# Performance work log

Hardware: AMD Instinct MI355X
Metric: run time of the kernel (lower is better)

## Reference

```python
import jax, jax.numpy as jnp
import numpy as np
from jax import lax

EMBED = 200
HID = 300
NCLASS = 2
B = 64
S = 255          # complete binary tree: 2**8 - 1 nodes
DEPTH = 8        # levels 0..7, root at node 0
VOCAB = 32000


def make_tree():
    parent = np.zeros(S, np.int32)
    parent[0] = S  # sentinel: root has no parent (dropped via dummy segment)
    for i in range(1, S):
        parent[i] = (i - 1) // 2
    depth = np.floor(np.log2(np.arange(S) + 1)).astype(np.int32)
    return jnp.asarray(parent), jnp.asarray(depth)


def setup_inputs() -> dict:
    key = jax.random.key(0)
    ks = jax.random.split(key, 8)
    parent, depth = make_tree()
    return {
        "x": jax.random.randint(ks[0], (S, B), 0, VOCAB, dtype=jnp.int32),
        "parent": parent,
        "depth": depth,
        "embed": jax.random.normal(ks[1], (VOCAB, EMBED), jnp.float32) * 0.1,
        "W_iou": jax.random.normal(ks[2], (EMBED, 3 * HID), jnp.float32) * 0.05,
        "U_iou": jax.random.normal(ks[3], (HID, 3 * HID), jnp.float32) * 0.05,
        "b_iou": jnp.zeros((3 * HID,), jnp.float32),
        "W_f": jax.random.normal(ks[4], (EMBED, HID), jnp.float32) * 0.05,
        "U_f": jax.random.normal(ks[5], (HID, HID), jnp.float32) * 0.05,
        "b_f": jnp.zeros((HID,), jnp.float32),
        "W_out": jax.random.normal(ks[6], (HID, NCLASS), jnp.float32) * 0.05,
        "b_out": jnp.zeros((NCLASS,), jnp.float32),
    }


def reference(x, parent, depth, embed, W_iou, U_iou, b_iou, W_f, U_f, b_f, W_out, b_out):
    # x: [S, B] token ids (seq-major, as in the torch model)
    emb = embed[x]                              # [S, B, E]
    wx_iou = emb @ W_iou + b_iou                # [S, B, 3H] input contributions
    wx_f = emb @ W_f + b_f                      # [S, B, H]
    seg = jnp.minimum(parent, S)                # root -> dummy segment S
    pidx = jnp.clip(parent, 0, S - 1)           # safe gather index for parent's x-part

    H0 = jnp.zeros((S, B, HID), emb.dtype)
    C0 = jnp.zeros((S, B, HID), emb.dtype)

    def level_step(carry, d):
        H, C = carry
        child = (depth == d + 1)[:, None, None].astype(H.dtype)   # nodes feeding level d
        # child-sum of hidden states into parents
        h_sum = jax.ops.segment_sum(H * child, seg, num_segments=S + 1)[:S]  # [S,B,H]
        # per-child forget gate: sigma(W_f x_parent + U_f h_child + b_f)
        f = jax.nn.sigmoid(wx_f[pidx] + H @ U_f)                  # [S,B,H]
        fc = jax.ops.segment_sum(f * C * child, seg, num_segments=S + 1)[:S]
        iou = wx_iou + h_sum @ U_iou                              # [S,B,3H]
        i_g, o_g, u_g = jnp.split(iou, 3, axis=-1)
        i_g = jax.nn.sigmoid(i_g)
        o_g = jax.nn.sigmoid(o_g)
        u_g = jnp.tanh(u_g)
        c_new = i_g * u_g + fc
        h_new = o_g * jnp.tanh(c_new)
        node = (depth == d)[:, None, None]
        H = jnp.where(node, h_new, H)
        C = jnp.where(node, c_new, C)
        return (H, C), None

    levels = jnp.arange(DEPTH - 1, -1, -1)      # process deepest level first
    (H, C), _ = lax.scan(level_step, (H0, C0), levels)

    tree_hidden = H[0]                          # [B, H] root hidden state
    logits = tree_hidden @ W_out + b_out        # Linear(hidden_dim, n_class)
    return jax.nn.log_softmax(logits, axis=-1)  # [B, 2]
```

## Files before the change

kernel.cpp:

```cpp
#include <hip/hip_runtime.h>
#include <hip/hip_bf16.h>
#include <math.h>

#define NS 255
#define NB 64
#define NE 200
#define NH 300
#define TS 2048


typedef __attribute__((ext_vector_type(8))) short short8;
typedef __attribute__((ext_vector_type(4))) float f32x4;

__device__ __forceinline__ float sigmoidf_(float x) { return 1.0f / (1.0f + __expf(-x)); }
__device__ __forceinline__ unsigned short f2bf(float v) {
    union { __hip_bfloat16 b; unsigned short u; } cv; cv.b = __float2bfloat16(v); return cv.u;
}
__device__ __forceinline__ float bf2f(unsigned short u) {
    union { unsigned short u; __hip_bfloat16 b; } cv; cv.u = u; return __bfloat162float(cv.b);
}
__device__ __forceinline__ int swz(int row, int kk) {
    int g = (kk >> 3) ^ ((row >> 1) & 3);
    return ((row << 2) + g) * 8 + (kk & 7);
}

__global__ __launch_bounds__(256) void prep_kernel(
    const float* __restrict__ U_iou, const float* __restrict__ U_f,
    const float* __restrict__ W_iou, const float* __restrict__ W_f,
    const float* __restrict__ embed, const int* __restrict__ x,
    unsigned short* __restrict__ BW, unsigned short* __restrict__ AembT)
{
    const int nBW = 4 * 5 * 17 * TS;
    const int nAe = NS * 7 * TS;
    int total = nBW + nAe;
    int stride = gridDim.x * blockDim.x;
    for (int i = blockIdx.x * blockDim.x + threadIdx.x; i < total; i += stride) {
        if (i < nBW) {
            int e = i & (TS - 1), tile = i >> 11;
            int c = tile % 17, t2 = tile / 17;
            int s = t2 % 5, g = t2 / 5;
            int row = e >> 5, pos = (e >> 3) & 3;
            int kk = ((pos ^ ((row >> 1) & 3)) << 3) + (e & 7);
            int j = s * 64 + row;
            float v = 0.f;
            if (c < 7) {
                int k = c * 32 + kk;
                if (j < NH && k < NE) v = (g < 3) ? W_iou[k * 900 + g * NH + j] : W_f[k * NH + j];
            } else {
                int k = (c - 7) * 32 + kk;
                if (j < NH && k < NH) v = (g < 3) ? U_iou[k * 900 + g * NH + j] : U_f[k * NH + j];
            }
            BW[i] = f2bf(v);
        } else {
            int i2 = i - nBW;
            int e = i2 & (TS - 1), tile = i2 >> 11;
            int c = tile % 7, node = tile / 7;
            int row = e >> 5, pos = (e >> 3) & 3;
            int kk = ((pos ^ ((row >> 1) & 3)) << 3) + (e & 7);
            int k = c * 32 + kk;
            float v = 0.f;
            if (k < NE) v = embed[(size_t)x[node * NB + row] * NE + k];
            AembT[i2] = f2bf(v);
        }
    }
}

template<int NCH>
__device__ __forceinline__ void gemm_h(f32x4 acc[4][2],
    const unsigned short* __restrict__ A, const unsigned short* __restrict__ B,
    int offA, int offB)
{
#pragma unroll
    for (int c = 0; c < NCH; ++c) {
        const unsigned short* At = A + c * TS + offA;
        const unsigned short* Bt = B + c * TS + offB;
        short8 a0 = *(const short8*)(At);
        short8 a1 = *(const short8*)(At + 512);
#pragma unroll
        for (int t = 0; t < 4; ++t) {
            short8 b = *(const short8*)(Bt + t * 512);
            acc[t][0] = __builtin_amdgcn_mfma_f32_16x16x32_bf16(a0, b, acc[t][0], 0, 0, 0);
            acc[t][1] = __builtin_amdgcn_mfma_f32_16x16x32_bf16(a1, b, acc[t][1], 0, 0, 0);
        }
    }
}

__global__ __launch_bounds__(320) void level_kernel(
    const unsigned short* __restrict__ AembT, const unsigned short* __restrict__ BW,
    const float* __restrict__ b_iou, const float* __restrict__ b_f,
    unsigned short* __restrict__ HbfT, float* __restrict__ C,
    int base, int m, int sh)
{
    int bid = blockIdx.x;
    int p, s, half;
    if (m > 0) {
        int xcd = bid & 7, idx = bid >> 3;
        int o = idx % m, rest = idx / m;
        p = base + xcd * m + o;
        s = rest % 5; half = rest / 5;
    } else {
        int xcd = bid & 7;
        if (xcd & ((1 << sh) - 1)) return;
        p = base + (xcd >> sh);
        int idx = bid >> 3;
        s = idx % 5; half = idx / 5;
    }
    int tid = threadIdx.x;
    int w = tid >> 6, lane = tid & 63, ln = lane & 15, quad = lane >> 4;
    int l = 2 * p + 1, r = 2 * p + 2;
    int bsel = (w < 4) ? w : 3;
    int g = (quad ^ ((ln >> 1) & 3)) * 8;
    int offA = (half * 32 + ln) * 32 + g;
    int offB = ln * 32 + g;

    const unsigned short* Bsrc = BW + (size_t)(bsel * 5 + s) * 17 * TS;
    const unsigned short* Ae = AembT + (size_t)p * 7 * TS;
    const unsigned short* Hl = HbfT + (size_t)l * 10 * TS;
    const unsigned short* Hr = HbfT + (size_t)r * 10 * TS;

    f32x4 acc[4][2];
#pragma unroll
    for (int t = 0; t < 4; ++t)
#pragma unroll
        for (int q = 0; q < 2; ++q) acc[t][q] = (f32x4){0.f, 0.f, 0.f, 0.f};

    if (w < 3) {
        gemm_h<7>(acc, Ae, Bsrc, offA, offB);
        gemm_h<10>(acc, Hl, Bsrc + 7 * TS, offA, offB);
        gemm_h<10>(acc, Hr, Bsrc + 7 * TS, offA, offB);
    } else {
        gemm_h<7>(acc, Ae, Bsrc, offA, offB);
        gemm_h<10>(acc, (w == 3) ? Hl : Hr, Bsrc + 7 * TS, offA, offB);
    }

    __shared__ float tile[5][32][17];
    for (int t = 0; t < 4; ++t) {
        __syncthreads();
#pragma unroll
        for (int ms = 0; ms < 2; ++ms)
#pragma unroll
            for (int rr = 0; rr < 4; ++rr)
                tile[w][ms * 16 + quad * 4 + rr][ln] = acc[t][ms][rr];
        __syncthreads();
        for (int idx = tid; idx < 512; idx += 320) {
            int mm = idx >> 4, n = idx & 15;
            int gm = half * 32 + mm;
            int jj = s * 64 + t * 16 + n;
            bool ok = jj < NH;
            float pi = tile[0][mm][n] + (ok ? b_iou[jj] : 0.f);
            float po = tile[1][mm][n] + (ok ? b_iou[NH + jj] : 0.f);
            float pu = tile[2][mm][n] + (ok ? b_iou[2 * NH + jj] : 0.f);
            float bj = ok ? b_f[jj] : 0.f;
            float fl = sigmoidf_(tile[3][mm][n] + bj);
            float fr = sigmoidf_(tile[4][mm][n] + bj);
            float cl = ok ? C[((size_t)l * NB + gm) * NH + jj] : 0.f;
            float cr = ok ? C[((size_t)r * NB + gm) * NH + jj] : 0.f;
            float cc = sigmoidf_(pi) * tanhf(pu) + fl * cl + fr * cr;
            float hh = sigmoidf_(po) * tanhf(cc);
            if (ok) C[((size_t)p * NB + gm) * NH + jj] = cc;
            HbfT[((size_t)p * 10 + (jj >> 5)) * TS + swz(gm, jj & 31)]
                = ok ? f2bf(hh) : (unsigned short)0;
        }
    }
}

__global__ __launch_bounds__(192) void leaf_kernel(
    const unsigned short* __restrict__ AembT, const unsigned short* __restrict__ BW,
    const float* __restrict__ b_iou,
    unsigned short* __restrict__ HbfT, float* __restrict__ C, int m)
{
    int bid = blockIdx.x;
    int xcd = bid & 7, idx = bid >> 3;
    int o = idx % m, rest = idx / m;
    int p = 127 + xcd * m + o;
    int s = rest % 5, half = rest / 5;
    int tid = threadIdx.x;
    int w = tid >> 6, lane = tid & 63, ln = lane & 15, quad = lane >> 4;
    int g = (quad ^ ((ln >> 1) & 3)) * 8;
    int offA = (half * 32 + ln) * 32 + g;
    int offB = ln * 32 + g;

    const unsigned short* Bsrc = BW + (size_t)(w * 5 + s) * 17 * TS;
    const unsigned short* Ae = AembT + (size_t)p * 7 * TS;

    f32x4 acc[4][2];
#pragma unroll
    for (int t = 0; t < 4; ++t)
#pragma unroll
        for (int q = 0; q < 2; ++q) acc[t][q] = (f32x4){0.f, 0.f, 0.f, 0.f};

    gemm_h<7>(acc, Ae, Bsrc, offA, offB);

    __shared__ float tile[3][32][17];
    for (int t = 0; t < 4; ++t) {
        __syncthreads();
#pragma unroll
        for (int ms = 0; ms < 2; ++ms)
#pragma unroll
            for (int rr = 0; rr < 4; ++rr)
                tile[w][ms * 16 + quad * 4 + rr][ln] = acc[t][ms][rr];
        __syncthreads();
        for (int idx2 = tid; idx2 < 512; idx2 += 192) {
            int mm = idx2 >> 4, n = idx2 & 15;
            int gm = half * 32 + mm;
            int jj = s * 64 + t * 16 + n;
            bool ok = jj < NH;
            float pi = tile[0][mm][n] + (ok ? b_iou[jj] : 0.f);
            float po = tile[1][mm][n] + (ok ? b_iou[NH + jj] : 0.f);
            float pu = tile[2][mm][n] + (ok ? b_iou[2 * NH + jj] : 0.f);
            float cc = sigmoidf_(pi) * tanhf(pu);
            float hh = sigmoidf_(po) * tanhf(cc);
            if (ok) C[((size_t)p * NB + gm) * NH + jj] = cc;
            HbfT[((size_t)p * 10 + (jj >> 5)) * TS + swz(gm, jj & 31)]
                = ok ? f2bf(hh) : (unsigned short)0;
        }
    }
}

__global__ __launch_bounds__(64) void out_kernel(
    const unsigned short* __restrict__ HbfT,
    const float* __restrict__ W_out, const float* __restrict__ b_out,
    float* __restrict__ out)
{
    int b = threadIdx.x;
    float l0 = 0.f, l1 = 0.f;
#pragma unroll 4
    for (int k = 0; k < NH; ++k) {
        float hk = bf2f(HbfT[(size_t)(k >> 5) * TS + swz(b, k & 31)]);
        l0 += hk * W_out[k * 2];
        l1 += hk * W_out[k * 2 + 1];
    }
    l0 += b_out[0];
    l1 += b_out[1];
    float m = fmaxf(l0, l1);
    float lse = m + logf(__expf(l0 - m) + __expf(l1 - m));
    out[b * 2 + 0] = l0 - lse;
    out[b * 2 + 1] = l1 - lse;
}

extern "C" void kernel_launch(void* const* d_in, const int* in_sizes, int n_in,
                              void* d_out, int out_size, void* d_ws, size_t ws_size,
                              hipStream_t stream)
{
    const int*   x     = (const int*)d_in[0];
    const float* embed = (const float*)d_in[3];
    const float* W_iou = (const float*)d_in[4];
    const float* U_iou = (const float*)d_in[5];
    const float* b_iou = (const float*)d_in[6];
    const float* W_f   = (const float*)d_in[7];
    const float* U_f   = (const float*)d_in[8];
    const float* b_f   = (const float*)d_in[9];
    const float* W_out = (const float*)d_in[10];
    const float* b_out = (const float*)d_in[11];

    char* ws = (char*)d_ws;
    unsigned short* HbfT  = (unsigned short*)(ws + 0);
    float*          C     = (float*)(ws + 10444800);
    unsigned short* AembT = (unsigned short*)(ws + 30028800);
    unsigned short* BW    = (unsigned short*)(ws + 37340160);

    prep_kernel<<<4096, 256, 0, stream>>>(U_iou, U_f, W_iou, W_f, embed, x, BW, AembT);

    leaf_kernel<<<1280, 192, 0, stream>>>(AembT, BW, b_iou, HbfT, C, 16);
    for (int d = 6; d >= 3; --d) {
        int base = (1 << d) - 1;
        int m = 1 << (d - 3);
        level_kernel<<<80 * m, 320, 0, stream>>>(AembT, BW, b_iou, b_f, HbfT, C,
                                                 base, m, 0);
    }
    for (int d = 2; d >= 0; --d) {
        level_kernel<<<80, 320, 0, stream>>>(AembT, BW, b_iou, b_f, HbfT, C,
                                             (1 << d) - 1, 0, 3 - d);
    }
    out_kernel<<<1, 64, 0, stream>>>(HbfT, W_out, b_out, (float*)d_out);
}
```

Baseline: 289.2 us.

## Fuse all tree levels into one persistent kernel with global atomic barriers

Replaces the prep, leaf, per-level and output launches with a single persistent kernel of 512 blocks that synchronises between phases using atomic-counter grid barriers. The prep phase now writes eight bf16 values per thread as vector stores. The leaf phase processes all 64 batch rows per block using a wider 4x4 MFMA accumulator. The aim is to remove the launch overhead and tail gaps of nine separate kernels. In exchange it depends on all 512 blocks being co-resident, spins on atomics, and leaves most blocks idle in the upper tree levels.

Result: slower. 696.2 us (+140.8%).

```diff
diff --git a/kernel.cpp b/kernel.cpp
--- a/kernel.cpp
+++ b/kernel.cpp
@@ -7,6 +7,7 @@
 #define NE 200
 #define NH 300
 #define TS 2048
+#define NBLK 512
 
 
 typedef __attribute__((ext_vector_type(8))) short short8;
@@ -24,45 +25,15 @@
     return ((row << 2) + g) * 8 + (kk & 7);
 }
 
-__global__ __launch_bounds__(256) void prep_kernel(
-    const float* __restrict__ U_iou, const float* __restrict__ U_f,
-    const float* __restrict__ W_iou, const float* __restrict__ W_f,
-    const float* __restrict__ embed, const int* __restrict__ x,
-    unsigned short* __restrict__ BW, unsigned short* __restrict__ AembT)
-{
-    const int nBW = 4 * 5 * 17 * TS;
-    const int nAe = NS * 7 * TS;
-    int total = nBW + nAe;
-    int stride = gridDim.x * blockDim.x;
-    for (int i = blockIdx.x * blockDim.x + threadIdx.x; i < total; i += stride) {
-        if (i < nBW) {
-            int e = i & (TS - 1), tile = i >> 11;
-            int c = tile % 17, t2 = tile / 17;
-            int s = t2 % 5, g = t2 / 5;
-            int row = e >> 5, pos = (e >> 3) & 3;
-            int kk = ((pos ^ ((row >> 1) & 3)) << 3) + (e & 7);
-            int j = s * 64 + row;
-            float v = 0.f;
-            if (c < 7) {
-                int k = c * 32 + kk;
-                if (j < NH && k < NE) v = (g < 3) ? W_iou[k * 900 + g * NH + j] : W_f[k * NH + j];
-            } else {
-                int k = (c - 7) * 32 + kk;
-                if (j < NH && k < NH) v = (g < 3) ? U_iou[k * 900 + g * NH + j] : U_f[k * NH + j];
-            }
-            BW[i] = f2bf(v);
-        } else {
-            int i2 = i - nBW;
-            int e = i2 & (TS - 1), tile = i2 >> 11;
-            int c = tile % 7, node = tile / 7;
-            int row = e >> 5, pos = (e >> 3) & 3;
-            int kk = ((pos ^ ((row >> 1) & 3)) << 3) + (e & 7);
-            int k = c * 32 + kk;
-            float v = 0.f;
-            if (k < NE) v = embed[(size_t)x[node * NB + row] * NE + k];
-            AembT[i2] = f2bf(v);
-        }
-    }
+__device__ __forceinline__ void gbar(int* c, int tid) {
+    __syncthreads();
+    if (tid == 0) {
+        __builtin_amdgcn_fence(__ATOMIC_RELEASE, "agent");
+        __hip_atomic_fetch_add(c, 1, __ATOMIC_RELAXED, __HIP_MEMORY_SCOPE_AGENT);
+        while (__hip_atomic_load(c, __ATOMIC_RELAXED, __HIP_MEMORY_SCOPE_AGENT) < NBLK)
+            __builtin_amdgcn_s_sleep(2);
+    }
+    __syncthreads();
 }
 
 template<int NCH>
@@ -84,28 +55,36 @@
         }
     }
 }
-
-__global__ __launch_bounds__(320) void level_kernel(
-    const unsigned short* __restrict__ AembT, const unsigned short* __restrict__ BW,
+template<int NCH>
+__device__ __forceinline__ void gemm_f(f32x4 acc[4][4],
+    const unsigned short* __restrict__ A, const unsigned short* __restrict__ B,
+    int off)
+{
+#pragma unroll
+    for (int c = 0; c < NCH; ++c) {
+        const unsigned short* At = A + c * TS + off;
+        const unsigned short* Bt = B + c * TS + off;
+        short8 a0 = *(const short8*)(At);
+        short8 a1 = *(const short8*)(At + 512);
+        short8 a2 = *(const short8*)(At + 1024);
+        short8 a3 = *(const short8*)(At + 1536);
+#pragma unroll
+        for (int t = 0; t < 4; ++t) {
+            short8 b = *(const short8*)(Bt + t * 512);
+            acc[t][0] = __builtin_amdgcn_mfma_f32_16x16x32_bf16(a0, b, acc[t][0], 0, 0, 0);
+            acc[t][1] = __builtin_amdgcn_mfma_f32_16x16x32_bf16(a1, b, acc[t][1], 0, 0, 0);
+            acc[t][2] = __builtin_amdgcn_mfma_f32_16x16x32_bf16(a2, b, acc[t][2], 0, 0, 0);
+            acc[t][3] = __builtin_amdgcn_mfma_f32_16x16x32_bf16(a3, b, acc[t][3], 0, 0, 0);
+        }
+    }
+}
+
+__device__ __forceinline__ void do_internal(float* smf, int p, int s, int half,
+    int tid, const unsigned short* __restrict__ AembT,
+    const unsigned short* __restrict__ BW,
     const float* __restrict__ b_iou, const float* __restrict__ b_f,
-    unsigned short* __restrict__ HbfT, float* __restrict__ C,
-    int base, int m, int sh)
-{
-    int bid = blockIdx.x;
-    int p, s, half;
-    if (m > 0) {
-        int xcd = bid & 7, idx = bid >> 3;
-        int o = idx % m, rest = idx / m;
-        p = base + xcd * m + o;
-        s = rest % 5; half = rest / 5;
-    } else {
-        int xcd = bid & 7;
-        if (xcd & ((1 << sh) - 1)) return;
-        p = base + (xcd >> sh);
-        int idx = bid >> 3;
-        s = idx % 5; half = idx / 5;
-    }
-    int tid = threadIdx.x;
+    unsigned short* __restrict__ HbfT, float* __restrict__ C)
+{
     int w = tid >> 6, lane = tid & 63, ln = lane & 15, quad = lane >> 4;
     int l = 2 * p + 1, r = 2 * p + 2;
     int bsel = (w < 4) ? w : 3;
@@ -133,26 +112,25 @@
         gemm_h<10>(acc, (w == 3) ? Hl : Hr, Bsrc + 7 * TS, offA, offB);
     }
 
-    __shared__ float tile[5][32][17];
     for (int t = 0; t < 4; ++t) {
         __syncthreads();
 #pragma unroll
         for (int ms = 0; ms < 2; ++ms)
 #pragma unroll
             for (int rr = 0; rr < 4; ++rr)
-                tile[w][ms * 16 + quad * 4 + rr][ln] = acc[t][ms][rr];
+                smf[w * 544 + (ms * 16 + quad * 4 + rr) * 17 + ln] = acc[t][ms][rr];
         __syncthreads();
         for (int idx = tid; idx < 512; idx += 320) {
             int mm = idx >> 4, n = idx & 15;
             int gm = half * 32 + mm;
             int jj = s * 64 + t * 16 + n;
             bool ok = jj < NH;
-            float pi = tile[0][mm][n] + (ok ? b_iou[jj] : 0.f);
-            float po = tile[1][mm][n] + (ok ? b_iou[NH + jj] : 0.f);
-            float pu = tile[2][mm][n] + (ok ? b_iou[2 * NH + jj] : 0.f);
+            float pi = smf[0 * 544 + mm * 17 + n] + (ok ? b_iou[jj] : 0.f);
+            float po = smf[1 * 544 + mm * 17 + n] + (ok ? b_iou[NH + jj] : 0.f);
+            float pu = smf[2 * 544 + mm * 17 + n] + (ok ? b_iou[2 * NH + jj] : 0.f);
             float bj = ok ? b_f[jj] : 0.f;
-            float fl = sigmoidf_(tile[3][mm][n] + bj);
-            float fr = sigmoidf_(tile[4][mm][n] + bj);
+            float fl = sigmoidf_(smf[3 * 544 + mm * 17 + n] + bj);
+            float fr = sigmoidf_(smf[4 * 544 + mm * 17 + n] + bj);
             float cl = ok ? C[((size_t)l * NB + gm) * NH + jj] : 0.f;
             float cr = ok ? C[((size_t)r * NB + gm) * NH + jj] : 0.f;
             float cc = sigmoidf_(pi) * tanhf(pu) + fl * cl + fr * cr;
@@ -164,91 +142,171 @@
     }
 }
 
-__global__ __launch_bounds__(192) void leaf_kernel(
-    const unsigned short* __restrict__ AembT, const unsigned short* __restrict__ BW,
-    const float* __restrict__ b_iou,
-    unsigned short* __restrict__ HbfT, float* __restrict__ C, int m)
-{
-    int bid = blockIdx.x;
-    int xcd = bid & 7, idx = bid >> 3;
-    int o = idx % m, rest = idx / m;
-    int p = 127 + xcd * m + o;
-    int s = rest % 5, half = rest / 5;
-    int tid = threadIdx.x;
+__device__ __forceinline__ void do_leaf(float* smf, int p, int s,
+    int tid, const unsigned short* __restrict__ AembT,
+    const unsigned short* __restrict__ BW, const float* __restrict__ b_iou,
+    unsigned short* __restrict__ HbfT, float* __restrict__ C)
+{
     int w = tid >> 6, lane = tid & 63, ln = lane & 15, quad = lane >> 4;
-    int g = (quad ^ ((ln >> 1) & 3)) * 8;
-    int offA = (half * 32 + ln) * 32 + g;
-    int offB = ln * 32 + g;
-
-    const unsigned short* Bsrc = BW + (size_t)(w * 5 + s) * 17 * TS;
-    const unsigned short* Ae = AembT + (size_t)p * 7 * TS;
-
-    f32x4 acc[4][2];
+    int off = ln * 32 + (quad ^ ((ln >> 1) & 3)) * 8;
+
+    f32x4 acc[4][4];
 #pragma unroll
     for (int t = 0; t < 4; ++t)
 #pragma unroll
-        for (int q = 0; q < 2; ++q) acc[t][q] = (f32x4){0.f, 0.f, 0.f, 0.f};
-
-    gemm_h<7>(acc, Ae, Bsrc, offA, offB);
-
-    __shared__ float tile[3][32][17];
+        for (int q = 0; q < 4; ++q) acc[t][q] = (f32x4){0.f, 0.f, 0.f, 0.f};
+
+    if (w < 3) {
+        const unsigned short* Bsrc = BW + (size_t)(w * 5 + s) * 17 * TS;
+        const unsigned short* Ae = AembT + (size_t)p * 7 * TS;
+        gemm_f<7>(acc, Ae, Bsrc, off);
+    }
+
     for (int t = 0; t < 4; ++t) {
         __syncthreads();
-#pragma unroll
-        for (int ms = 0; ms < 2; ++ms)
-#pragma unroll
-            for (int rr = 0; rr < 4; ++rr)
-                tile[w][ms * 16 + quad * 4 + rr][ln] = acc[t][ms][rr];
+        if (w < 3)
+#pragma unroll
+            for (int ms = 0; ms < 4; ++ms)
+#pragma unroll
+                for (int rr = 0; rr < 4; ++rr)
+                    smf[w * 1024 + (ms * 16 + quad * 4 + rr) * 16 + ln] = acc[t][ms][rr];
         __syncthreads();
-        for (int idx2 = tid; idx2 < 512; idx2 += 192) {
-            int mm = idx2 >> 4, n = idx2 & 15;
-            int gm = half * 32 + mm;
+        for (int idx = tid; idx < 1024; idx += 320) {
+            int mm = idx >> 4, n = idx & 15;
             int jj = s * 64 + t * 16 + n;
             bool ok = jj < NH;
-            float pi = tile[0][mm][n] + (ok ? b_iou[jj] : 0.f);
-            float po = tile[1][mm][n] + (ok ? b_iou[NH + jj] : 0.f);
-            float pu = tile[2][mm][n] + (ok ? b_iou[2 * NH + jj] : 0.f);
+            float pi = smf[0 * 1024 + mm * 16 + n] + (ok ? b_iou[jj] : 0.f);
+            float po = smf[1 * 1024 + mm * 16 + n] + (ok ? b_iou[NH + jj] : 0.f);
+            float pu = smf[2 * 1024 + mm * 16 + n] + (ok ? b_iou[2 * NH + jj] : 0.f);
             float cc = sigmoidf_(pi) * tanhf(pu);
             float hh = sigmoidf_(po) * tanhf(cc);
-            if (ok) C[((size_t)p * NB + gm) * NH + jj] = cc;
-            HbfT[((size_t)p * 10 + (jj >> 5)) * TS + swz(gm, jj & 31)]
+            if (ok) C[((size_t)p * NB + mm) * NH + jj] = cc;
+            HbfT[((size_t)p * 10 + (jj >> 5)) * TS + swz(mm, jj & 31)]
                 = ok ? f2bf(hh) : (unsigned short)0;
         }
     }
 }
 
-__global__ __launch_bounds__(64) void out_kernel(
-    const unsigned short* __restrict__ HbfT,
+__global__ __launch_bounds__(320, 4) void fused_kernel(
+    const float* __restrict__ U_iou, const float* __restrict__ U_f,
+    const float* __restrict__ W_iou, const float* __restrict__ W_f,
+    const float* __restrict__ embed, const int* __restrict__ x,
+    const float* __restrict__ b_iou, const float* __restrict__ b_f,
     const float* __restrict__ W_out, const float* __restrict__ b_out,
-    float* __restrict__ out)
-{
-    int b = threadIdx.x;
-    float l0 = 0.f, l1 = 0.f;
+    unsigned short* __restrict__ BW, unsigned short* __restrict__ AembT,
+    unsigned short* __restrict__ HbfT, float* __restrict__ C,
+    float* __restrict__ out, int* __restrict__ bar)
+{
+    __shared__ float smf[3072];
+    int bid = blockIdx.x;
+    int tid = threadIdx.x;
+
+    {
+        const int gBW = 4 * 5 * 17 * 256;
+        const int gAe = NS * 7 * 256;
+        int total = gBW + gAe;
+        int stride = NBLK * 320;
+        for (int gi = bid * 320 + tid; gi < total; gi += stride) {
+            unsigned short st[8];
+            if (gi < gBW) {
+                int gg = gi & 255, tile = gi >> 8;
+                int row = gg >> 2, pos = gg & 3;
+                int kk0 = (pos ^ ((row >> 1) & 3)) << 3;
+                int c = tile % 17, t2 = tile / 17;
+                int s = t2 % 5, g4 = t2 / 5;
+                int j = s * 64 + row;
+#pragma unroll
+                for (int u = 0; u < 8; ++u) {
+                    int kk = kk0 + u; float v = 0.f;
+                    if (c < 7) {
+                        int k = c * 32 + kk;
+                        if (j < NH && k < NE)
+                            v = (g4 < 3) ? W_iou[k * 900 + g4 * NH + j] : W_f[k * NH + j];
+                    } else {
+                        int k = (c - 7) * 32 + kk;
+                        if (j < NH && k < NH)
+                            v = (g4 < 3) ? U_iou[k * 900 + g4 * NH + j] : U_f[k * NH + j];
+                    }
+                    st[u] = f2bf(v);
+                }
+                *(short8*)(BW + (size_t)tile * TS + (row * 4 + pos) * 8) = *(short8*)st;
+            } else {
+                int gi2 = gi - gBW;
+                int gg = gi2 & 255, tile = gi2 >> 8;
+                int row = gg >> 2, pos = gg & 3;
+                int kk0 = (pos ^ ((row >> 1) & 3)) << 3;
+                int c = tile % 7, node = tile / 7;
+                int k0 = c * 32 + kk0;
+                const float* er = embed + (size_t)x[node * NB + row] * NE;
+#pragma unroll
+                for (int u = 0; u < 8; ++u)
+                    st[u] = (k0 + u < NE) ? f2bf(er[k0 + u]) : (unsigned short)0;
+                *(short8*)(AembT + (size_t)tile * TS + (row * 4 + pos) * 8) = *(short8*)st;
+            }
+        }
+    }
+    gbar(bar + 0, tid);
+
+    int xcd = bid & 7, slot = bid >> 3;
+
+    for (int t = slot; t < 80; t += 64) {
+        int o = t % 16, s = t / 16;
+        do_leaf(smf, 127 + xcd * 16 + o, s, tid, AembT, BW, b_iou, HbfT, C);
+    }
+    gbar(bar + 1, tid);
+
+    int bi = 2;
+    for (int d = 6; d >= 3; --d) {
+        int base = (1 << d) - 1;
+        int m = 1 << (d - 3);
+        int T = m * 10;
+        for (int t = slot; t < T; t += 64) {
+            int o = t % m, rest = t / m;
+            do_internal(smf, base + xcd * m + o, rest % 5, rest / 5,
+                        tid, AembT, BW, b_iou, b_f, HbfT, C);
+        }
+        gbar(bar + bi++, tid);
+    }
+    for (int d = 2; d >= 0; --d) {
+        int n = 1 << d;
+        int sh = 3 - d;
+        if ((xcd & ((1 << sh) - 1)) == 0 && (xcd >> sh) < n && slot < 10) {
+            int idx = xcd >> sh;
+            do_internal(smf, n - 1 + idx, slot % 5, slot / 5,
+                        tid, AembT, BW, b_iou, b_f, HbfT, C);
+        }
+        gbar(bar + bi++, tid);
+    }
+
+    if (bid == 0 && tid < NB) {
+        int b = tid;
+        float l0 = 0.f, l1 = 0.f;
 #pragma unroll 4
-    for (int k = 0; k < NH; ++k) {
-        float hk = bf2f(HbfT[(size_t)(k >> 5) * TS + swz(b, k & 31)]);
-        l0 += hk * W_out[k * 2];
-        l1 += hk * W_out[k * 2 + 1];
-    }
-    l0 += b_out[0];
-    l1 += b_out[1];
-    float m = fmaxf(l0, l1);
-    float lse = m + logf(__expf(l0 - m) + __expf(l1 - m));
-    out[b * 2 + 0] = l0 - lse;
-    out[b * 2 + 1] = l1 - lse;
+        for (int k = 0; k < NH; ++k) {
+            float hk = bf2f(HbfT[(size_t)(k >> 5) * TS + swz(b, k & 31)]);
+            l0 += hk * W_out[k * 2];
+            l1 += hk * W_out[k * 2 + 1];
+        }
+        l0 += b_out[0];
+        l1 += b_out[1];
+        float mx = fmaxf(l0, l1);
+        float lse = mx + logf(__expf(l0 - mx) + __expf(l1 - mx));
+        out[b * 2 + 0] = l0 - lse;
+        out[b * 2 + 1] = l1 - lse;
+    }
 }
 
 extern "C" void kernel_launch(void* const* d_in, const int* in_sizes, int n_in,
                               void* d_out, int out_size, void* d_ws, size_t ws_size,
                               hipStream_t stream)
 {
+    const float* U_iou = (const float*)d_in[5];
+    const float* U_f   = (const float*)d_in[8];
+    const float* W_iou = (const float*)d_in[4];
+    const float* W_f   = (const float*)d_in[7];
+    const float* embed = (const float*)d_in[3];
     const int*   x     = (const int*)d_in[0];
-    const float* embed = (const float*)d_in[3];
-    const float* W_iou = (const float*)d_in[4];
-    const float* U_iou = (const float*)d_in[5];
     const float* b_iou = (const float*)d_in[6];
-    const float* W_f   = (const float*)d_in[7];
-    const float* U_f   = (const float*)d_in[8];
     const float* b_f   = (const float*)d_in[9];
     const float* W_out = (const float*)d_in[10];
     const float* b_out = (const float*)d_in[11];
@@ -258,19 +316,11 @@
     float*          C     = (float*)(ws + 10444800);
     unsigned short* AembT = (unsigned short*)(ws + 30028800);
     unsigned short* BW    = (unsigned short*)(ws + 37340160);
-
-    prep_kernel<<<4096, 256, 0, stream>>>(U_iou, U_f, W_iou, W_f, embed, x, BW, AembT);
-
-    leaf_kernel<<<1280, 192, 0, stream>>>(AembT, BW, b_iou, HbfT, C, 16);
-    for (int d = 6; d >= 3; --d) {
-        int base = (1 << d) - 1;
-        int m = 1 << (d - 3);
-        level_kernel<<<80 * m, 320, 0, stream>>>(AembT, BW, b_iou, b_f, HbfT, C,
-                                                 base, m, 0);
-    }
-    for (int d = 2; d >= 0; --d) {
-        level_kernel<<<80, 320, 0, stream>>>(AembT, BW, b_iou, b_f, HbfT, C,
-                                             (1 << d) - 1, 0, 3 - d);
-    }
-    out_kernel<<<1, 64, 0, stream>>>(HbfT, W_out, b_out, (float*)d_out);
-}
+    int*            bar   = (int*)(ws + 38732800);
+
+    hipMemsetAsync(bar, 0, 64, stream);
+    fused_kernel<<<NBLK, 320, 0, stream>>>(U_iou, U_f, W_iou, W_f, embed, x,
+                                           b_iou, b_f, W_out, b_out,
+                                           BW, AembT, HbfT, C,
+                                           (float*)d_out, bar);
+}
```
